# Kernel optimization log

Hardware: AMD Instinct MI355X
Metric: run time of the kernel (lower is better)

## Reference

```python
import jax, jax.numpy as jnp
import numpy as np

SHARPNESS = 2


def setup_inputs() -> dict:
    key = jax.random.key(0)
    k1, k2, k3 = jax.random.split(key, 3)
    x = jax.random.normal(k1, (16, 256, 48, 48), dtype=jnp.float32)
    # 1x1 conv == per-pixel linear: weight (out_c, in_c), bias (out_c,)
    W = jax.random.normal(k2, (256, 256), dtype=jnp.float32) * 0.0625
    bias = jax.random.normal(k3, (256,), dtype=jnp.float32) * 0.01
    return {"x": x, "W": W, "bias": bias}


def reference(x, W, bias):
    b, c, h, w = x.shape
    hw = h * w
    # sample-wide L2 norm over the full (c*h*w) vector (faithful to source)
    xn = jnp.linalg.norm(x.reshape(b, -1), axis=1).reshape(b, 1, 1)
    # NOTE: raw reshapes of the (b,c,h,w)-contiguous tensor, NOT transposes
    x1 = x.reshape(b, hw, c) / xn
    x2 = x.reshape(b, c, hw) / xn
    cos = jnp.einsum('bnc,bcm->bnm', x1, x2)          # (b, hw, hw)
    s = jnp.maximum(cos, 0.0) ** SHARPNESS            # relu^sharpness
    # transform block: 1x1 conv
    tr = jnp.einsum('oc,bchw->bohw', W, x) + bias[None, :, None, None]
    tr = tr.reshape(b, hw, c)                         # raw reshape, as in source
    y = jnp.einsum('bnm,bmc->bnc', s, tr)             # (b, hw, c)
    return y.reshape(b, c, h, w)
```

## Files before the change

### kernel.cpp

```cpp
#include <hip/hip_runtime.h>

#define NB 16
#define NC 256
#define HW 2304
#define CHW 589824

typedef __attribute__((ext_vector_type(8))) short bf16x8;
typedef __attribute__((ext_vector_type(16))) float f32x16;

union BF8 { bf16x8 v; unsigned short u[8]; unsigned d[4]; };

__device__ inline unsigned short f2bf(float f) {
  unsigned u = __builtin_bit_cast(unsigned, f);
  u += 0x7fffu + ((u >> 16) & 1u);
  return (unsigned short)(u >> 16);
}

__device__ inline unsigned f2bf2(float lo, float hi) {
  unsigned r;
  asm("v_cvt_pk_bf16_f32 %0, %1, %2" : "=v"(r) : "v"(lo), "v"(hi));
  return r;
}

__global__ __launch_bounds__(256) void prep_kernel(const float* __restrict__ x,
                                                   const float* __restrict__ W,
                                                   unsigned short* __restrict__ wp,
                                                   unsigned short* __restrict__ xtp,
                                                   double* __restrict__ partials) {
  __shared__ __align__(16) char smem[33344];
  const int bid = blockIdx.x;
  const int tid = threadIdx.x;

  if (bid < 8) {
    const int rt = bid;
    float* tile = (float*)smem;
    const float4* src = (const float4*)(W + (size_t)rt * 32 * 256);
    #pragma unroll
    for (int it = 0; it < 8; ++it) {
      const int i = tid + 256 * it;
      float4 v = src[i];
      const int fi = 4 * i, row = fi >> 8, col = fi & 255;
      *(float4*)&tile[row * 260 + col] = v;
    }
    __syncthreads();
    const int w = tid >> 6, l = tid & 63, l31 = l & 31, h = l >> 5;
    unsigned short* dst = wp + (size_t)rt * 8192;
    #pragma unroll
    for (int ff = 0; ff < 4; ++ff) {
      const int f = 4 * w + ff;
      const float* rp = &tile[l31 * 260 + 16 * f + 8 * h];
      const float4 r0 = *(const float4*)rp;
      const float4 r1 = *(const float4*)(rp + 4);
      BF8 o;
      o.d[0] = f2bf2(r0.x, r0.y);
      o.d[1] = f2bf2(r0.z, r0.w);
      o.d[2] = f2bf2(r1.x, r1.y);
      o.d[3] = f2bf2(r1.z, r1.w);
      *(bf16x8*)(dst + (((size_t)f) * 64 + l) * 8) = o.v;
    }
  } else {
    const int e = bid - 8;
    const int mt = e % 36, kt = (e / 36) % 4, b = e / 144;
    const int m0 = mt * 64, k0 = kt * 64;
    float* tile = (float*)smem;
    double* red = (double*)(smem + 17408);
    const float* xb = x + (size_t)b * CHW;
    double ss = 0.0;
    #pragma unroll
    for (int it = 0; it < 4; ++it) {
      const int i = tid + 256 * it;
      const int row = i >> 4, c4 = (i & 15) * 4;
      float4 v = *(const float4*)(xb + (size_t)(k0 + row) * HW + m0 + c4);
      *(float4*)&tile[row * 68 + c4] = v;
      ss += (double)v.x * v.x + (double)v.y * v.y + (double)v.z * v.z + (double)v.w * v.w;
    }
    #pragma unroll
    for (int off = 32; off > 0; off >>= 1) ss += __shfl_down(ss, off, 64);
    const int w = tid >> 6, l = tid & 63;
    if (l == 0) red[w] = ss;
    __syncthreads();
    if (tid == 0) partials[b * 144 + kt * 36 + mt] = red[0] + red[1] + red[2] + red[3];
    const int l31 = l & 31, h = l >> 5;
    unsigned short* dst = xtp + (size_t)b * CHW;
    #pragma unroll
    for (int pp = 0; pp < 2; ++pp) {
      const int p = 2 * w + pp, mbl = p >> 2, fl = p & 3;
      BF8 o;
      #pragma unroll
      for (int jj = 0; jj < 4; ++jj) {
        const float e0 = tile[(16 * fl + 8 * h + 2 * jj) * 68 + 32 * mbl + l31];
        const float e1 = tile[(16 * fl + 8 * h + 2 * jj + 1) * 68 + 32 * mbl + l31];
        o.d[jj] = f2bf2(e0, e1);
      }
      const int mb = 2 * mt + mbl, f = 4 * kt + fl;
      *(bf16x8*)(dst + (((size_t)mb * 16 + f) * 64 + l) * 8) = o.v;
    }
  }
}

__global__ __launch_bounds__(192) void conv3_kernel(const unsigned short* __restrict__ wp,
                                                    const float* __restrict__ bias,
                                                    const unsigned short* __restrict__ xtp,
                                                    unsigned short* __restrict__ trp,
                                                    const double* __restrict__ partials,
                                                    float* __restrict__ inv_xn2) {
  const int bid = blockIdx.x;
  if (bid == 1024) {
    const int t = threadIdx.x;
    if (t >= 128) return;
    const int b = t >> 3, i0 = t & 7;
    double v = 0.0;
    for (int i = i0; i < 144; i += 8) v += partials[b * 144 + i];
    v += __shfl_down(v, 4, 64);
    v += __shfl_down(v, 2, 64);
    v += __shfl_down(v, 1, 64);
    if (i0 == 0) inv_xn2[b] = (float)(1.0 / v);
    return;
  }
  const int xcd = bid & 7, r = bid >> 3;
  const int b = xcd + 8 * (r & 1);
  const int r2 = r >> 1;
  const int rt = r2 >> 3, cb8 = r2 & 7;
  const int tid = threadIdx.x, w = tid >> 6, l = tid & 63, l31 = l & 31, h = l >> 5;
  const unsigned short* xb = xtp + (size_t)b * CHW;

  __shared__ unsigned short tile[32 * 296];

  bf16x8 af[16];
  #pragma unroll
  for (int f = 0; f < 16; ++f)
    af[f] = *(const bf16x8*)(wp + (((size_t)rt * 16 + f) * 64 + l) * 8);
  float bcol[16];
  #pragma unroll
  for (int reg = 0; reg < 16; ++reg) {
    const int rowl = (reg & 3) + 8 * (reg >> 2) + 4 * h;
    bcol[reg] = bias[32 * rt + rowl];
  }

  #pragma unroll
  for (int si = 0; si < 3; ++si) {
    const int s = 3 * w + si;
    const int mb = 8 * s + cb8;
    f32x16 acc;
    #pragma unroll
    for (int rr = 0; rr < 16; ++rr) acc[rr] = 0.f;
    #pragma unroll
    for (int f = 0; f < 16; ++f) {
      bf16x8 bv = *(const bf16x8*)(xb + (((size_t)mb * 16 + f) * 64 + l) * 8);
      acc = __builtin_amdgcn_mfma_f32_32x32x16_bf16(af[f], bv, acc, 0, 0, 0);
    }
    #pragma unroll
    for (int p = 0; p < 8; ++p) {
      const int r0 = 2 * p, r1 = 2 * p + 1;
      const int rowl = (r0 & 3) + 8 * (r0 >> 2) + 4 * h;
      const unsigned pk = f2bf2(acc[r0] + bcol[r0], acc[r1] + bcol[r1]);
      tile[rowl * 296 + 32 * s + l31] = (unsigned short)pk;
      tile[(rowl + 1) * 296 + 32 * s + l31] = (unsigned short)(pk >> 16);
    }
  }
  __syncthreads();

  unsigned short* tb = trp + (size_t)b * CHW;
  #pragma unroll
  for (int si = 0; si < 6; ++si) {
    const int kfi = 6 * w + si;
    const int mbase = 288 * rt + 16 * kfi;
    const int mb2 = mbase >> 6, kf = (mbase >> 4) & 3;
    BF8 o;
    #pragma unroll
    for (int j = 0; j < 8; ++j) {
      const int m = mbase + 8 * h + j;
      const int a = m / 9, s = m - 9 * a;
      o.u[j] = tile[(a - 32 * rt) * 296 + 32 * s + l31];
    }
    *(bf16x8*)(tb + (size_t)mb2 * 16384 + (((size_t)cb8 * 4 + kf) * 64 + l) * 8) = o.v;
  }
}

#define CHUNK_BODY(CH, CUR, NXT)                                                                   \
  {                                                                                                \
    const int ch_ = (CH);                                                                          \
    const int pb_ = ch_ & 1;                                                                       \
    f32x16 s0, s1;                                                                                 \
    _Pragma("unroll")                                                                              \
    for (int i = 0; i < 16; ++i) { s0[i] = 0.f; s1[i] = 0.f; }                                     \
    _Pragma("unroll")                                                                              \
    for (int f = 0; f < 16; ++f) {                                                                 \
      bf16x8 a0 = *(const bf16x8*)(Af + f * 512 + lane * 8);                                       \
      bf16x8 a1 = *(const bf16x8*)(Af + (16 + f) * 512 + lane * 8);                                \
      s0 = __builtin_amdgcn_mfma_f32_32x32x16_bf16(a0, CUR[f], s0, 0, 0, 0);                       \
      s1 = __builtin_amdgcn_mfma_f32_32x32x16_bf16(a1, CUR[f], s1, 0, 0, 0);                       \
    }                                                                                              \
    bf16x8 bt0[8], bt1[8];                                                                         \
    _Pragma("unroll")                                                                              \
    for (int kk = 0; kk < 8; ++kk) {                                                               \
      const size_t mb_ = 2 * ch_ + (kk >> 2);                                                      \
      bt0[kk] = *(const bf16x8*)(ttb + mb_ * 16384 + ((size_t)((2 * c) * 4 + (kk & 3))) * 512 + lane * 8);     \
      bt1[kk] = *(const bf16x8*)(ttb + mb_ * 16384 + ((size_t)((2 * c + 1) * 4 + (kk & 3))) * 512 + lane * 8); \
    }                                                                                              \
    _Pragma("unroll")                                                                              \
    for (int reg = 0; reg < 16; ++reg) {                                                           \
      const int rowp = (reg & 3) + 8 * (reg >> 2) + 4 * h;                                         \
      float v0 = fmaxf(s0[reg] * inv2, 0.f); v0 *= v0;                                             \
      float v1 = fmaxf(s1[reg] * inv2, 0.f); v1 *= v1;                                             \
      Pl[pb_][rowp][32 * c + l31] = f2bf(v0);                                                      \
      Pl[pb_][32 + rowp][32 * c + l31] = f2bf(v1);                                                 \
    }                                                                                              \
    const int chn_ = (ch_ < 17) ? ch_ + 1 : 17;                                                    \
    const unsigned short* bpn_ = xtb + (size_t)((4 * chn_ + c) * 16) * 512 + lane * 8;             \
    _Pragma("unroll")                                                                              \
    for (int f = 0; f < 16; ++f) NXT[f] = *(const bf16x8*)(bpn_ + f * 512);                        \
    __syncthreads();                                                                               \
    _Pragma("unroll")                                                                              \
    for (int kk = 0; kk < 8; ++kk) {                                                               \
      bf16x8 pf0 = *(const bf16x8*)&Pl[pb_][l31][16 * kk + 8 * h];                                 \
      bf16x8 pf1 = *(const bf16x8*)&Pl[pb_][32 + l31][16 * kk + 8 * h];                            \
      yacc[0][0] = __builtin_amdgcn_mfma_f32_32x32x16_bf16(pf0, bt0[kk], yacc[0][0], 0, 0, 0);     \
      yacc[1][0] = __builtin_amdgcn_mfma_f32_32x32x16_bf16(pf1, bt0[kk], yacc[1][0], 0, 0, 0);     \
      yacc[0][1] = __builtin_amdgcn_mfma_f32_32x32x16_bf16(pf0, bt1[kk], yacc[0][1], 0, 0, 0);     \
      yacc[1][1] = __builtin_amdgcn_mfma_f32_32x32x16_bf16(pf1, bt1[kk], yacc[1][1], 0, 0, 0);     \
    }                                                                                              \
  }

__global__ __launch_bounds__(256, 2) void fused_kernel(const float* __restrict__ x,
                                                       const unsigned short* __restrict__ xtp,
                                                       const unsigned short* __restrict__ trp,
                                                       const float* __restrict__ inv_xn2,
                                                       float* __restrict__ out) {
  const int bid = blockIdx.x;
  const int xcd = bid & 7, j = bid >> 3;
  const int hi = (j >= 36) ? 1 : 0;
  const int b = xcd + 8 * hi;
  const int nt = j - 36 * hi;
  const float* xsrc = x + (size_t)b * CHW;
  const unsigned short* xtb = xtp + (size_t)b * CHW;
  const unsigned short* ttb = trp + (size_t)b * CHW;
  float* ob = out + (size_t)b * CHW;
  const float inv2 = inv_xn2[b];

  const int tid = threadIdx.x;
  const int c = tid >> 6, lane = tid & 63;
  const int l31 = lane & 31, h = lane >> 5;

  __shared__ unsigned short Af[16384];
  __shared__ unsigned short Pl[2][64][136];

  {
    #pragma unroll
    for (int it = 0; it < 8; ++it) {
      const int idx = tid + 256 * it;
      const int f = idx >> 6, l = idx & 63;
      const int ll31 = l & 31, hh = l >> 5;
      const float* sp = xsrc + (size_t)(64 * nt + 32 * (f >> 4) + ll31) * 256 + 16 * (f & 15) + 8 * hh;
      const float4 r0 = *(const float4*)sp;
      const float4 r1 = *(const float4*)(sp + 4);
      BF8 o;
      o.d[0] = f2bf2(r0.x, r0.y);
      o.d[1] = f2bf2(r0.z, r0.w);
      o.d[2] = f2bf2(r1.x, r1.y);
      o.d[3] = f2bf2(r1.z, r1.w);
      *(bf16x8*)(Af + (size_t)f * 512 + (size_t)l * 8) = o.v;
    }
  }

  bf16x8 bva[16], bvb[16];
  {
    const unsigned short* bp0 = xtb + (size_t)(c * 16) * 512 + lane * 8;
    #pragma unroll
    for (int f = 0; f < 16; ++f) bva[f] = *(const bf16x8*)(bp0 + f * 512);
  }
  __syncthreads();

  f32x16 yacc[2][2];
  #pragma unroll
  for (int nh = 0; nh < 2; ++nh)
    #pragma unroll
    for (int cb = 0; cb < 2; ++cb)
      #pragma unroll
      for (int i = 0; i < 16; ++i) yacc[nh][cb][i] = 0.f;

  for (int ci = 0; ci < 9; ++ci) {
    CHUNK_BODY(2 * ci, bva, bvb)
    CHUNK_BODY(2 * ci + 1, bvb, bva)
  }

  #pragma unroll
  for (int nh = 0; nh < 2; ++nh)
    #pragma unroll
    for (int cb = 0; cb < 2; ++cb) {
      const int col = 64 * c + 32 * cb + l31;
      #pragma unroll
      for (int reg = 0; reg < 16; ++reg) {
        const int rowp = (reg & 3) + 8 * (reg >> 2) + 4 * h;
        ob[(size_t)(64 * nt + 32 * nh + rowp) * NC + col] = yacc[nh][cb][reg];
      }
    }
}

extern "C" void kernel_launch(void* const* d_in, const int* in_sizes, int n_in,
                              void* d_out, int out_size, void* d_ws, size_t ws_size,
                              hipStream_t stream) {
  const float* x    = (const float*)d_in[0];
  const float* W    = (const float*)d_in[1];
  const float* bias = (const float*)d_in[2];
  float* out = (float*)d_out;

  const size_t SZ = (size_t)NB * CHW * sizeof(unsigned short);
  double* partials       = (double*)d_ws;
  float* inv_xn2         = (float*)((char*)d_ws + 24576);
  unsigned short* wp     = (unsigned short*)((char*)d_ws + 32768);
  unsigned short* xtp    = (unsigned short*)((char*)d_ws + 163840 + SZ);
  unsigned short* trp    = (unsigned short*)((char*)d_ws + 163840 + 3 * SZ);

  prep_kernel<<<2312, 256, 0, stream>>>(x, W, wp, xtp, partials);
  conv3_kernel<<<1025, 192, 0, stream>>>(wp, bias, xtp, trp, partials, inv_xn2);
  fused_kernel<<<576, 256, 0, stream>>>(x, xtp, trp, inv_xn2, out);
}
```

Before: 234.2 us.

## Fold weight bf16 packing into conv kernel and widen conv blocks to 576 threads

Removes the separate W-to-bf16 packing blocks from the prep kernel. Each conv block now converts its W rows directly from fp32 into MFMA fragments. The conv kernel goes from 192 threads doing 3 tiles per wave to 576 threads doing one tile per wave, which spreads the MFMA and store work over more waves. The cost is redundant W conversion in every conv block and heavier register pressure and lower occupancy per block at 576 threads.

```diff
diff --git a/kernel.cpp b/kernel.cpp
--- a/kernel.cpp
+++ b/kernel.cpp
@@ -23,82 +23,49 @@
 }
 
 __global__ __launch_bounds__(256) void prep_kernel(const float* __restrict__ x,
-                                                   const float* __restrict__ W,
-                                                   unsigned short* __restrict__ wp,
                                                    unsigned short* __restrict__ xtp,
                                                    double* __restrict__ partials) {
-  __shared__ __align__(16) char smem[33344];
-  const int bid = blockIdx.x;
+  __shared__ __align__(16) char smem[17440];
+  const int e = blockIdx.x;
   const int tid = threadIdx.x;
-
-  if (bid < 8) {
-    const int rt = bid;
-    float* tile = (float*)smem;
-    const float4* src = (const float4*)(W + (size_t)rt * 32 * 256);
-    #pragma unroll
-    for (int it = 0; it < 8; ++it) {
-      const int i = tid + 256 * it;
-      float4 v = src[i];
-      const int fi = 4 * i, row = fi >> 8, col = fi & 255;
-      *(float4*)&tile[row * 260 + col] = v;
-    }
-    __syncthreads();
-    const int w = tid >> 6, l = tid & 63, l31 = l & 31, h = l >> 5;
-    unsigned short* dst = wp + (size_t)rt * 8192;
-    #pragma unroll
-    for (int ff = 0; ff < 4; ++ff) {
-      const int f = 4 * w + ff;
-      const float* rp = &tile[l31 * 260 + 16 * f + 8 * h];
-      const float4 r0 = *(const float4*)rp;
-      const float4 r1 = *(const float4*)(rp + 4);
-      BF8 o;
-      o.d[0] = f2bf2(r0.x, r0.y);
-      o.d[1] = f2bf2(r0.z, r0.w);
-      o.d[2] = f2bf2(r1.x, r1.y);
-      o.d[3] = f2bf2(r1.z, r1.w);
-      *(bf16x8*)(dst + (((size_t)f) * 64 + l) * 8) = o.v;
-    }
-  } else {
-    const int e = bid - 8;
-    const int mt = e % 36, kt = (e / 36) % 4, b = e / 144;
-    const int m0 = mt * 64, k0 = kt * 64;
-    float* tile = (float*)smem;
-    double* red = (double*)(smem + 17408);
-    const float* xb = x + (size_t)b * CHW;
-    double ss = 0.0;
-    #pragma unroll
-    for (int it = 0; it < 4; ++it) {
-      const int i = tid + 256 * it;
-      const int row = i >> 4, c4 = (i & 15) * 4;
-      float4 v = *(const float4*)(xb + (size_t)(k0 + row) * HW + m0 + c4);
-      *(float4*)&tile[row * 68 + c4] = v;
-      ss += (double)v.x * v.x + (double)v.y * v.y + (double)v.z * v.z + (double)v.w * v.w;
-    }
-    #pragma unroll
-    for (int off = 32; off > 0; off >>= 1) ss += __shfl_down(ss, off, 64);
-    const int w = tid >> 6, l = tid & 63;
-    if (l == 0) red[w] = ss;
-    __syncthreads();
-    if (tid == 0) partials[b * 144 + kt * 36 + mt] = red[0] + red[1] + red[2] + red[3];
-    const int l31 = l & 31, h = l >> 5;
-    unsigned short* dst = xtp + (size_t)b * CHW;
-    #pragma unroll
-    for (int pp = 0; pp < 2; ++pp) {
-      const int p = 2 * w + pp, mbl = p >> 2, fl = p & 3;
-      BF8 o;
-      #pragma unroll
-      for (int jj = 0; jj < 4; ++jj) {
-        const float e0 = tile[(16 * fl + 8 * h + 2 * jj) * 68 + 32 * mbl + l31];
-        const float e1 = tile[(16 * fl + 8 * h + 2 * jj + 1) * 68 + 32 * mbl + l31];
-        o.d[jj] = f2bf2(e0, e1);
-      }
-      const int mb = 2 * mt + mbl, f = 4 * kt + fl;
-      *(bf16x8*)(dst + (((size_t)mb * 16 + f) * 64 + l) * 8) = o.v;
-    }
-  }
-}
-
-__global__ __launch_bounds__(192) void conv3_kernel(const unsigned short* __restrict__ wp,
+  const int mt = e % 36, kt = (e / 36) % 4, b = e / 144;
+  const int m0 = mt * 64, k0 = kt * 64;
+  float* tile = (float*)smem;
+  double* red = (double*)(smem + 17408);
+  const float* xb = x + (size_t)b * CHW;
+  double ss = 0.0;
+  #pragma unroll
+  for (int it = 0; it < 4; ++it) {
+    const int i = tid + 256 * it;
+    const int row = i >> 4, c4 = (i & 15) * 4;
+    float4 v = *(const float4*)(xb + (size_t)(k0 + row) * HW + m0 + c4);
+    *(float4*)&tile[row * 68 + c4] = v;
+    ss += (double)v.x * v.x + (double)v.y * v.y + (double)v.z * v.z + (double)v.w * v.w;
+  }
+  #pragma unroll
+  for (int off = 32; off > 0; off >>= 1) ss += __shfl_down(ss, off, 64);
+  const int w = tid >> 6, l = tid & 63;
+  if (l == 0) red[w] = ss;
+  __syncthreads();
+  if (tid == 0) partials[b * 144 + kt * 36 + mt] = red[0] + red[1] + red[2] + red[3];
+  const int l31 = l & 31, h = l >> 5;
+  unsigned short* dst = xtp + (size_t)b * CHW;
+  #pragma unroll
+  for (int pp = 0; pp < 2; ++pp) {
+    const int p = 2 * w + pp, mbl = p >> 2, fl = p & 3;
+    BF8 o;
+    #pragma unroll
+    for (int jj = 0; jj < 4; ++jj) {
+      const float e0 = tile[(16 * fl + 8 * h + 2 * jj) * 68 + 32 * mbl + l31];
+      const float e1 = tile[(16 * fl + 8 * h + 2 * jj + 1) * 68 + 32 * mbl + l31];
+      o.d[jj] = f2bf2(e0, e1);
+    }
+    const int mb = 2 * mt + mbl, f = 4 * kt + fl;
+    *(bf16x8*)(dst + (((size_t)mb * 16 + f) * 64 + l) * 8) = o.v;
+  }
+}
+
+__global__ __launch_bounds__(576) void conv3_kernel(const float* __restrict__ W,
                                                     const float* __restrict__ bias,
                                                     const unsigned short* __restrict__ xtp,
                                                     unsigned short* __restrict__ trp,
@@ -127,9 +94,20 @@
   __shared__ unsigned short tile[32 * 296];
 
   bf16x8 af[16];
-  #pragma unroll
-  for (int f = 0; f < 16; ++f)
-    af[f] = *(const bf16x8*)(wp + (((size_t)rt * 16 + f) * 64 + l) * 8);
+  {
+    const float* wrow = W + (size_t)(32 * rt + l31) * 256 + 8 * h;
+    #pragma unroll
+    for (int f = 0; f < 16; ++f) {
+      const float4 r0 = *(const float4*)(wrow + 16 * f);
+      const float4 r1 = *(const float4*)(wrow + 16 * f + 4);
+      BF8 o;
+      o.d[0] = f2bf2(r0.x, r0.y);
+      o.d[1] = f2bf2(r0.z, r0.w);
+      o.d[2] = f2bf2(r1.x, r1.y);
+      o.d[3] = f2bf2(r1.z, r1.w);
+      af[f] = o.v;
+    }
+  }
   float bcol[16];
   #pragma unroll
   for (int reg = 0; reg < 16; ++reg) {
@@ -137,9 +115,8 @@
     bcol[reg] = bias[32 * rt + rowl];
   }
 
-  #pragma unroll
-  for (int si = 0; si < 3; ++si) {
-    const int s = 3 * w + si;
+  {
+    const int s = w;
     const int mb = 8 * s + cb8;
     f32x16 acc;
     #pragma unroll
@@ -162,8 +139,8 @@
 
   unsigned short* tb = trp + (size_t)b * CHW;
   #pragma unroll
-  for (int si = 0; si < 6; ++si) {
-    const int kfi = 6 * w + si;
+  for (int si = 0; si < 2; ++si) {
+    const int kfi = 2 * w + si;
     const int mbase = 288 * rt + 16 * kfi;
     const int mb2 = mbase >> 6, kf = (mbase >> 4) & 3;
     BF8 o;
@@ -308,11 +285,10 @@
   const size_t SZ = (size_t)NB * CHW * sizeof(unsigned short);
   double* partials       = (double*)d_ws;
   float* inv_xn2         = (float*)((char*)d_ws + 24576);
-  unsigned short* wp     = (unsigned short*)((char*)d_ws + 32768);
   unsigned short* xtp    = (unsigned short*)((char*)d_ws + 163840 + SZ);
   unsigned short* trp    = (unsigned short*)((char*)d_ws + 163840 + 3 * SZ);
 
-  prep_kernel<<<2312, 256, 0, stream>>>(x, W, wp, xtp, partials);
-  conv3_kernel<<<1025, 192, 0, stream>>>(wp, bias, xtp, trp, partials, inv_xn2);
+  prep_kernel<<<2304, 256, 0, stream>>>(x, xtp, partials);
+  conv3_kernel<<<1025, 576, 0, stream>>>(W, bias, xtp, trp, partials, inv_xn2);
   fused_kernel<<<576, 256, 0, stream>>>(x, xtp, trp, inv_xn2, out);
 }
```

New measurement: 251.5 us. 1.07x slower.
